# Optimization experiments

Measured on AMD Instinct MI355X. Metric: run time of the kernel, lower is better.

## Reference

```python
import jax, jax.numpy as jnp
import numpy as np

B, LQ, LK, E, H = 4, 2048, 2048, 768, 12
D = E // H  # head_dim = 64
SCALE = 0.25 / np.sqrt(D)
LN_EPS = 1e-5


def _layernorm(x, g, b):
    mu = jnp.mean(x, axis=-1, keepdims=True)
    var = jnp.mean(jnp.square(x - mu), axis=-1, keepdims=True)
    return (x - mu) * jax.lax.rsqrt(var + LN_EPS) * g + b


def _rope(x, f):
    # x: [B,H,L,D]; f: [L,D//2,2] (real, imag) -- complex multiply on interleaved pairs
    xr = x.reshape(*x.shape[:-1], D // 2, 2)
    fr = f[None, None]  # [1,1,L,D//2,2]
    real = xr[..., 0] * fr[..., 0] - xr[..., 1] * fr[..., 1]
    imag = xr[..., 0] * fr[..., 1] + xr[..., 1] * fr[..., 0]
    return jnp.stack([real, imag], axis=-1).reshape(x.shape)


def setup_inputs() -> dict:
    key = jax.random.key(0)
    ks = jax.random.split(key, 8)
    x_q = jax.random.normal(ks[0], (B, LQ, E), jnp.float32)
    x_kv = jax.random.normal(ks[1], (B, LK, E), jnp.float32)
    # unit-magnitude rotary tables (cos, sin of random angles)
    ang_q = jax.random.uniform(ks[2], (LQ, D // 2), jnp.float32, 0.0, 2 * np.pi)
    ang_k = jax.random.uniform(ks[3], (LK, D // 2), jnp.float32, 0.0, 2 * np.pi)
    freqs_cis = jnp.stack([jnp.cos(ang_q), jnp.sin(ang_q)], axis=-1)
    freqs_cis_cross = jnp.stack([jnp.cos(ang_k), jnp.sin(ang_k)], axis=-1)
    Wq = jax.random.normal(ks[4], (E, E), jnp.float32) * 0.02
    Wkv = jax.random.normal(ks[5], (E, 2 * E), jnp.float32) * 0.02
    Wo = jax.random.normal(ks[6], (E, E), jnp.float32) * 0.02
    bo = jnp.zeros((E,), jnp.float32)
    return {
        'x_q': x_q, 'x_kv': x_kv,
        'freqs_cis': freqs_cis, 'freqs_cis_cross': freqs_cis_cross,
        'Wq': Wq, 'Wkv': Wkv, 'Wo': Wo, 'bo': bo,
        'ln_q_g': jnp.ones((E,), jnp.float32), 'ln_q_b': jnp.zeros((E,), jnp.float32),
        'ln_kv_g': jnp.ones((E,), jnp.float32), 'ln_kv_b': jnp.zeros((E,), jnp.float32),
        'gain': jnp.array(1.0, jnp.float32),
    }


def reference(x_q, x_kv, freqs_cis, freqs_cis_cross, Wq, Wkv, Wo, bo,
              ln_q_g, ln_q_b, ln_kv_g, ln_kv_b, gain):
    q = _layernorm(x_q, ln_q_g, ln_q_b) @ Wq                 # [B,LQ,E]
    kv = _layernorm(x_kv, ln_kv_g, ln_kv_b) @ Wkv            # [B,LK,2E]
    k, v = jnp.split(kv, 2, axis=-1)
    # b l (h d) -> b h l d
    q = q.reshape(B, LQ, H, D).transpose(0, 2, 1, 3)
    k = k.reshape(B, LK, H, D).transpose(0, 2, 1, 3)
    v = v.reshape(B, LK, H, D).transpose(0, 2, 1, 3)
    q = _rope(q, freqs_cis)
    k = _rope(k, freqs_cis_cross)
    attn = jnp.einsum('bhqd,bhkd->bhqk', q, k) * SCALE       # full O(L^2) matrix
    attn = jax.nn.softmax(attn, axis=-1)
    out = jnp.einsum('bhqk,bhkd->bhqd', attn, v)
    out = out.transpose(0, 2, 1, 3).reshape(B, LQ, E)        # b h l d -> b l (h d)
    return gain * (out @ Wo + bo)
```

## Files before the change

kernel.cpp:

```cpp
#include <hip/hip_runtime.h>
#include <hip/hip_bf16.h>

#define B_ 4
#define LQ_ 2048
#define LK_ 2048
#define E_ 768
#define H_ 12
#define D_ 64
#define SCALE_ 0.03125f
#define QSCALE_ 0.04508422f

using short8 = __attribute__((ext_vector_type(8))) short;
using f32x4  = __attribute__((ext_vector_type(4))) float;
using f32x16 = __attribute__((ext_vector_type(16))) float;

__device__ inline unsigned short f2bf(float f) {
    union { float f; unsigned u; } v; v.f = f;
    unsigned r = (v.u + 0x7FFFu + ((v.u >> 16) & 1u)) >> 16;
    return (unsigned short)r;
}

__device__ inline unsigned pkbf(float a, float b) {
    union { float f; unsigned u; } x, y; x.f = a; y.f = b;
    return ((x.u + 0x8000u) >> 16) | ((y.u + 0x8000u) & 0xffff0000u);
}

__device__ inline unsigned pkcvt(float a, float b) {
    float2 p; p.x = a; p.y = b;
    __hip_bfloat162 pb = __float22bfloat162_rn(p);
    union { __hip_bfloat162 h; unsigned u; } c; c.h = pb;
    return c.u;
}

__device__ inline void gll16(const void* g, void* l) {
    __builtin_amdgcn_global_load_lds(
        (const __attribute__((address_space(1))) unsigned int*)g,
        (__attribute__((address_space(3))) unsigned int*)l, 16, 0, 0);
}

__global__ __launch_bounds__(256) void ln_tr_kernel(
    const float* __restrict__ xq, const float* __restrict__ xkv,
    const float* __restrict__ gq, const float* __restrict__ bq,
    const float* __restrict__ gk, const float* __restrict__ bk,
    unsigned short* __restrict__ yq, unsigned short* __restrict__ ykv,
    const float* __restrict__ Wq, const float* __restrict__ Wkv, const float* __restrict__ Wo,
    unsigned short* __restrict__ WqT, unsigned short* __restrict__ WkvT, unsigned short* __restrict__ WoT)
{
    __shared__ float tile[32][33];
    int bid = blockIdx.x;
    if (bid < 4096) {
        int wave = threadIdx.x >> 6, lane = threadIdx.x & 63;
        int row = bid * 4 + wave;
        const float* x; const float* g; const float* be; unsigned short* y;
        if (row < 8192) { x = xq; g = gq; be = bq; y = yq; }
        else { row -= 8192; x = xkv; g = gk; be = bk; y = ykv; }
        const float* xr = x + (size_t)row * E_;
        float4 v[3];
        float s = 0.f;
#pragma unroll
        for (int i = 0; i < 3; i++) {
            v[i] = *(const float4*)(xr + i * 256 + lane * 4);
            s += v[i].x + v[i].y + v[i].z + v[i].w;
        }
#pragma unroll
        for (int off = 32; off >= 1; off >>= 1) s += __shfl_xor(s, off);
        float mu = s * (1.0f / E_);
        float q = 0.f;
#pragma unroll
        for (int i = 0; i < 3; i++) {
            float dx = v[i].x - mu, dy = v[i].y - mu, dz = v[i].z - mu, dw = v[i].w - mu;
            q += dx * dx + dy * dy + dz * dz + dw * dw;
        }
#pragma unroll
        for (int off = 32; off >= 1; off >>= 1) q += __shfl_xor(q, off);
        float rstd = rsqrtf(q * (1.0f / E_) + 1e-5f);
        unsigned short* yr = y + (size_t)row * E_;
#pragma unroll
        for (int i = 0; i < 3; i++) {
            int c = i * 256 + lane * 4;
            float4 gv = *(const float4*)(g + c);
            float4 bv = *(const float4*)(be + c);
            ushort4 o;
            o.x = f2bf((v[i].x - mu) * rstd * gv.x + bv.x);
            o.y = f2bf((v[i].y - mu) * rstd * gv.y + bv.y);
            o.z = f2bf((v[i].z - mu) * rstd * gv.z + bv.z);
            o.w = f2bf((v[i].w - mu) * rstd * gv.w + bv.w);
            *(ushort4*)(yr + c) = o;
        }
        return;
    }
    int b2 = bid - 4096;
    int z = b2 / 1152;
    int rem = b2 - z * 1152;
    int bx = rem % 48, by = rem / 48;
    const float* in; unsigned short* out; int C;
    if (z == 0)      { in = Wq;  out = WqT;  C = E_; }
    else if (z == 1) { in = Wkv; out = WkvT; C = 2 * E_; }
    else             { in = Wo;  out = WoT;  C = E_; }
    int c0 = bx * 32, r0 = by * 32;
    if (c0 >= C) return;
    int tx = threadIdx.x & 31, ty = threadIdx.x >> 5;
#pragma unroll
    for (int i = 0; i < 32; i += 8)
        tile[ty + i][tx] = in[(size_t)(r0 + ty + i) * C + c0 + tx];
    __syncthreads();
#pragma unroll
    for (int i = 0; i < 32; i += 8)
        out[(size_t)(c0 + ty + i) * E_ + r0 + tx] = f2bf(tile[tx][ty + i]);
}

#define BN 128
#define BK 64
template<int BMT>
__device__ __forceinline__ void gemm_body(
    const unsigned short* __restrict__ A, const unsigned short* __restrict__ Bt,
    int K, int mode, int bm, int bn,
    unsigned short* __restrict__ outQ, const float* __restrict__ freqs,
    unsigned short* __restrict__ outK, unsigned short* __restrict__ outV,
    float* __restrict__ outF, const float* __restrict__ bo, const float* __restrict__ gain)
{
    constexpr int MT = (BMT == 128) ? 4 : 2;
    constexpr int SMEMN = (BMT == 128) ? 128 * 136 : (BMT * 64 + 128 * 64);
    __shared__ __align__(16) unsigned short smem[SMEMN];
    auto Asm = (unsigned short (*)[BK])smem;
    auto Bsm = (unsigned short (*)[BK])(smem + BMT * BK);

    int tid = threadIdx.x;
    int wave = tid >> 6, lane = tid & 63;
    int quad = lane >> 4, l16 = lane & 15;
    int waveM = (wave >> 1) * (MT * 16), waveN = (wave & 1) * 64;
    int ro = lane >> 3, cx = lane & 7;
    int sco = ((cx ^ ro) * 8);

    f32x4 acc[MT][4] = {};

    for (int k0 = 0; k0 < K; k0 += BK) {
        const unsigned short* Ag = A + (size_t)(bm + wave * (BMT / 4) + ro) * K + k0 + sco;
        const unsigned short* Bg = Bt + (size_t)(bn + wave * 32 + ro) * K + k0 + sco;
#pragma unroll
        for (int i = 0; i < BMT / 32; i++)
            gll16(Ag + (size_t)(i * 8) * K, &Asm[wave * (BMT / 4) + i * 8][0]);
#pragma unroll
        for (int i = 0; i < 4; i++)
            gll16(Bg + (size_t)(i * 8) * K, &Bsm[wave * 32 + i * 8][0]);
        __syncthreads();
#pragma unroll
        for (int kk = 0; kk < BK; kk += 32) {
            short8 fa[MT], fb[4];
#pragma unroll
            for (int t = 0; t < 4; t++) {
                int pos = ((quad + (kk >> 3)) ^ (l16 & 7)) * 8;
                if (t < MT) fa[t] = *(const short8*)(&Asm[waveM + t * 16 + l16][pos]);
                fb[t] = *(const short8*)(&Bsm[waveN + t * 16 + l16][pos]);
            }
#pragma unroll
            for (int mt = 0; mt < MT; mt++)
#pragma unroll
                for (int nt = 0; nt < 4; nt++)
                    acc[mt][nt] = __builtin_amdgcn_mfma_f32_16x16x32_bf16(fa[mt], fb[nt], acc[mt][nt], 0, 0, 0);
        }
        __syncthreads();
    }

    if (BMT == 128 && mode == 1 && bn >= E_) {
        auto T = (unsigned short (*)[136])smem;
#pragma unroll
        for (int mt = 0; mt < MT; mt++) {
#pragma unroll
            for (int nt = 0; nt < 4; nt++) {
                int ml = waveM + mt * 16 + quad * 4;
                int nl = waveN + nt * 16 + l16;
                *(unsigned*)&T[nl][ml]     = pkbf(acc[mt][nt][0], acc[mt][nt][1]);
                *(unsigned*)&T[nl][ml + 2] = pkbf(acc[mt][nt][2], acc[mt][nt][3]);
            }
        }
        __syncthreads();
        int nnbase = bn - E_;
        int bb = bm >> 11, l0 = bm & (LQ_ - 1);
#pragma unroll
        for (int it = 0; it < 8; it++) {
            int row = it * 16 + (tid >> 4);
            int hh = (nnbase + row) >> 6, dd = (nnbase + row) & 63;
            short8 v = *(const short8*)&T[row][(tid & 15) * 8];
            *(short8*)(outV + (((size_t)bb * H_ + hh) * D_ + dd) * LK_ + l0 + (tid & 15) * 8) = v;
        }
        return;
    }

    float gg = (mode == 2) ? gain[0] : 0.f;
#pragma unroll
    for (int mt = 0; mt < MT; mt++) {
#pragma unroll
        for (int nt = 0; nt < 4; nt++) {
#pragma unroll
            for (int r = 0; r < 4; r++) {
                int m = bm + waveM + mt * 16 + quad * 4 + r;
                int n = bn + waveN + nt * 16 + l16;
                float v = acc[mt][nt][r];
                if (mode == 2) {
                    outF[(size_t)m * E_ + n] = gg * (v + bo[n]);
                } else {
                    int l = m & (LQ_ - 1), bb = m >> 11;
                    float partner = __shfl_xor(v, 1);
                    int h = n >> 6, dd = n & 63;
                    const float* f = freqs + ((size_t)l * 32 + (dd >> 1)) * 2;
                    float f0 = f[0], f1 = f[1];
                    float o = ((dd & 1) == 0) ? (v * f0 - partner * f1)
                                              : (partner * f1 + v * f0);
                    if (mode == 0) o *= QSCALE_;
                    unsigned short* dst = (mode == 0) ? outQ : outK;
                    dst[(((size_t)bb * H_ + h) * LQ_ + l) * D_ + dd] = f2bf(o);
                }
            }
        }
    }
}

template<int BMT>
__global__ __launch_bounds__(256) void gemm_kernel(
    const unsigned short* __restrict__ A, const unsigned short* __restrict__ Bt,
    int K, int mode,
    unsigned short* __restrict__ outQ, const float* __restrict__ freqs,
    unsigned short* __restrict__ outK, unsigned short* __restrict__ outV,
    float* __restrict__ outF, const float* __restrict__ bo, const float* __restrict__ gain)
{
    gemm_body<BMT>(A, Bt, K, mode, blockIdx.x * BMT, blockIdx.y * BN,
                   outQ, freqs, outK, outV, outF, bo, gain);
}

__global__ __launch_bounds__(256) void proj_kernel(
    const unsigned short* __restrict__ xq_ln, const unsigned short* __restrict__ xkv_ln,
    const unsigned short* __restrict__ WqT, const unsigned short* __restrict__ WkvT,
    unsigned short* __restrict__ Qb, unsigned short* __restrict__ Kb,
    unsigned short* __restrict__ Vt,
    const float* __restrict__ freqs_q, const float* __restrict__ freqs_k)
{
    int bid = blockIdx.x;
    const unsigned short* A; const unsigned short* Bt; int mode, bm, bn;
    const float* fr; unsigned short* oQ; unsigned short* oK; unsigned short* oV;
    if (bid < 768) {
        int x = bid & 63, y = bid >> 6;
        A = xkv_ln; Bt = WkvT; mode = 1; bm = x * 128; bn = y * 128;
        fr = freqs_k; oQ = nullptr; oK = Kb; oV = Vt;
    } else {
        int b2 = bid - 768;
        int x = b2 & 63, y = b2 >> 6;
        A = xq_ln; Bt = WqT; mode = 0; bm = x * 128; bn = y * 128;
        fr = freqs_q; oQ = Qb; oK = nullptr; oV = nullptr;
    }
    gemm_body<128>(A, Bt, E_, mode, bm, bn, oQ, fr, oK, oV, nullptr, nullptr, nullptr);
}

__global__ __launch_bounds__(256, 4) void attn_kernel(
    const unsigned short* __restrict__ Qg, const unsigned short* __restrict__ Kg,
    const unsigned short* __restrict__ Vt, unsigned short* __restrict__ O)
{
    __shared__ unsigned short Ksm[3][64][64];
    __shared__ unsigned short Vsm[3][64][64];

    int tid = threadIdx.x;
    int wave = tid >> 6, lane = tid & 63;
    int l32 = lane & 31, hi = lane >> 5;
    int bh = blockIdx.x;
    int b = bh / H_, h = bh % H_;
    int qbase = blockIdx.y * 128 + wave * 32;

    const size_t head = (size_t)bh * LK_ * D_;
    const unsigned short* Qh = Qg + head;
    const unsigned short* Kh = Kg + head;
    const unsigned short* Vh = Vt + head;

    short8 qf[4];
#pragma unroll
    for (int dc = 0; dc < 4; dc++)
        qf[dc] = *(const short8*)(Qh + (size_t)(qbase + l32) * D_ + dc * 16 + hi * 8);

    f32x16 oacc[2] = {};
    float lsum = 0.f;

    int ro = lane >> 3, cx = lane & 7;
    int sco = ((cx ^ ro) * 8);
    int sw = l32 & 7;

    auto stage = [&](int t, int bf) {
        const unsigned short* Kp = Kh + (size_t)(t * 64 + wave * 16 + ro) * D_ + sco;
        const unsigned short* Vp = Vh + (size_t)(wave * 16 + ro) * LK_ + t * 64 + sco;
        gll16(Kp,            &Ksm[bf][wave * 16][0]);
        gll16(Kp + 8 * D_,   &Ksm[bf][wave * 16 + 8][0]);
        gll16(Vp,            &Vsm[bf][wave * 16][0]);
        gll16(Vp + 8 * LK_,  &Vsm[bf][wave * 16 + 8][0]);
    };

    auto compute = [&](int bf) {
        f32x16 st0 = {}, st1 = {};
        __builtin_amdgcn_s_setprio(1);
#pragma unroll
        for (int dc = 0; dc < 4; dc++) {
            int pos = ((dc * 2 + hi) ^ sw) * 8;
            short8 k0 = *(const short8*)(&Ksm[bf][l32][pos]);
            short8 k1 = *(const short8*)(&Ksm[bf][32 + l32][pos]);
            st0 = __builtin_amdgcn_mfma_f32_32x32x16_bf16(k0, qf[dc], st0, 0, 0, 0);
            st1 = __builtin_amdgcn_mfma_f32_32x32x16_bf16(k1, qf[dc], st1, 0, 0, 0);
        }
        __builtin_amdgcn_s_setprio(0);

        unsigned pks0[8], pks1[8];
#pragma unroll
        for (int t = 0; t < 8; t++) {
            float p0 = __builtin_amdgcn_exp2f(st0[2 * t]);
            float p1 = __builtin_amdgcn_exp2f(st0[2 * t + 1]);
            lsum += p0 + p1;
            pks0[t] = pkcvt(p0, p1);
        }
#pragma unroll
        for (int t = 0; t < 8; t++) {
            float p0 = __builtin_amdgcn_exp2f(st1[2 * t]);
            float p1 = __builtin_amdgcn_exp2f(st1[2 * t + 1]);
            lsum += p0 + p1;
            pks1[t] = pkcvt(p0, p1);
        }
        asm("v_permlane32_swap_b32 %0, %1" : "+v"(pks0[0]), "+v"(pks0[2]));
        asm("v_permlane32_swap_b32 %0, %1" : "+v"(pks0[1]), "+v"(pks0[3]));
        asm("v_permlane32_swap_b32 %0, %1" : "+v"(pks0[4]), "+v"(pks0[6]));
        asm("v_permlane32_swap_b32 %0, %1" : "+v"(pks0[5]), "+v"(pks0[7]));
        asm("v_permlane32_swap_b32 %0, %1" : "+v"(pks1[0]), "+v"(pks1[2]));
        asm("v_permlane32_swap_b32 %0, %1" : "+v"(pks1[1]), "+v"(pks1[3]));
        asm("v_permlane32_swap_b32 %0, %1" : "+v"(pks1[4]), "+v"(pks1[6]));
        asm("v_permlane32_swap_b32 %0, %1" : "+v"(pks1[5]), "+v"(pks1[7]));

        __builtin_amdgcn_s_setprio(1);
#pragma unroll
        for (int half = 0; half < 2; half++) {
#pragma unroll
            for (int kk = 0; kk < 2; kk++) {
                union { unsigned u[4]; short8 s8; } pf;
#pragma unroll
                for (int g = 0; g < 4; g++)
                    pf.u[g] = half ? pks1[kk * 4 + g] : pks0[kk * 4 + g];
#pragma unroll
                for (int dt = 0; dt < 2; dt++) {
                    int pos = (((half * 2 + kk) * 2 + hi) ^ sw) * 8;
                    short8 vfr = *(const short8*)(&Vsm[bf][dt * 32 + l32][pos]);
                    oacc[dt] = __builtin_amdgcn_mfma_f32_32x32x16_bf16(pf.s8, vfr, oacc[dt], 0, 0, 0);
                }
            }
        }
        __builtin_amdgcn_s_setprio(0);
    };

    stage(0, 0);
    stage(1, 1);
    asm volatile("s_waitcnt vmcnt(4)\ns_barrier" ::: "memory");

    for (int t = 0; t < 30; ++t) {
        stage(t + 2, (t + 2) % 3);
        compute(t % 3);
        asm volatile("s_waitcnt vmcnt(4) lgkmcnt(0)\ns_barrier" ::: "memory");
    }
    compute(0);
    asm volatile("s_waitcnt vmcnt(0) lgkmcnt(0)\ns_barrier" ::: "memory");
    compute(1);

    lsum += __shfl_xor(lsum, 32);
    float inv = 1.f / lsum;
#pragma unroll
    for (int reg = 0; reg < 16; reg++) {
        int ql = (reg & 3) + 8 * (reg >> 2) + 4 * hi;
        float iq = __shfl(inv, ql);
        int q = qbase + ql;
        size_t base = ((size_t)b * LQ_ + q) * E_ + h * D_;
#pragma unroll
        for (int dt = 0; dt < 2; dt++)
            O[base + dt * 32 + l32] = f2bf(oacc[dt][reg] * iq);
    }
}

extern "C" void kernel_launch(void* const* d_in, const int* in_sizes, int n_in,
                              void* d_out, int out_size, void* d_ws, size_t ws_size,
                              hipStream_t stream)
{
    const float* x_q     = (const float*)d_in[0];
    const float* x_kv    = (const float*)d_in[1];
    const float* freqs_q = (const float*)d_in[2];
    const float* freqs_k = (const float*)d_in[3];
    const float* Wq      = (const float*)d_in[4];
    const float* Wkv     = (const float*)d_in[5];
    const float* Wo      = (const float*)d_in[6];
    const float* bo      = (const float*)d_in[7];
    const float* ln_q_g  = (const float*)d_in[8];
    const float* ln_q_b  = (const float*)d_in[9];
    const float* ln_kv_g = (const float*)d_in[10];
    const float* ln_kv_b = (const float*)d_in[11];
    const float* gain    = (const float*)d_in[12];
    float* out = (float*)d_out;

    unsigned short* ws = (unsigned short*)d_ws;
    const size_t SZ = (size_t)B_ * LQ_ * E_;
    unsigned short* xq_ln  = ws;
    unsigned short* xkv_ln = xq_ln + SZ;
    unsigned short* Qb     = xkv_ln + SZ;
    unsigned short* Kb     = Qb + SZ;
    unsigned short* Vt     = Kb + SZ;
    unsigned short* Ob     = xq_ln;
    unsigned short* WqT    = Vt + SZ;
    unsigned short* WkvT   = WqT + E_ * E_;
    unsigned short* WoT    = WkvT + 2 * E_ * E_;

    ln_tr_kernel<<<7552, 256, 0, stream>>>(x_q, x_kv, ln_q_g, ln_q_b, ln_kv_g, ln_kv_b,
                                           xq_ln, xkv_ln, Wq, Wkv, Wo, WqT, WkvT, WoT);
    proj_kernel<<<1152, 256, 0, stream>>>(xq_ln, xkv_ln, WqT, WkvT, Qb, Kb, Vt,
                                          freqs_q, freqs_k);
    attn_kernel<<<dim3(48, 16), 256, 0, stream>>>(Qb, Kb, Vt, Ob);
    gemm_kernel<64><<<dim3(128, 6), 256, 0, stream>>>(Ob, WoT, E_, 2,
                                                      nullptr, nullptr, nullptr, nullptr, out, bo, gain);
}
```

Baseline: 254.5 us.

## Compute softmax row sums with an MFMA against ones and unroll the triple-buffer loop

Drops the per-element VALU accumulation of the softmax denominator. The row sum is now produced by one extra MFMA per P fragment, multiplying the bf16 P against a vector of ones, which also removes the final shuffles. The K-tile loop is unrolled by three so buffer indices become compile-time constants, and LDS read offsets are precomputed. This costs one extra MFMA per 4 and a 16-register accumulator, and the sum now uses bf16-rounded P, which is consistent with the P·V numerator.

```diff
diff --git a/kernel.cpp b/kernel.cpp
--- a/kernel.cpp
+++ b/kernel.cpp
@@ -13,6 +13,8 @@
 using short8 = __attribute__((ext_vector_type(8))) short;
 using f32x4  = __attribute__((ext_vector_type(4))) float;
 using f32x16 = __attribute__((ext_vector_type(16))) float;
+
+template<int N> struct IC { static constexpr int v = N; };
 
 __device__ inline unsigned short f2bf(float f) {
     union { float f; unsigned u; } v; v.f = f;
@@ -255,8 +257,7 @@
     const unsigned short* __restrict__ Qg, const unsigned short* __restrict__ Kg,
     const unsigned short* __restrict__ Vt, unsigned short* __restrict__ O)
 {
-    __shared__ unsigned short Ksm[3][64][64];
-    __shared__ unsigned short Vsm[3][64][64];
+    __shared__ __align__(16) unsigned short smem[3 * 4096 * 2];
 
     int tid = threadIdx.x;
     int wave = tid >> 6, lane = tid & 63;
@@ -276,29 +277,43 @@
         qf[dc] = *(const short8*)(Qh + (size_t)(qbase + l32) * D_ + dc * 16 + hi * 8);
 
     f32x16 oacc[2] = {};
-    float lsum = 0.f;
+    f32x16 lacc = {};
+
+    short8 ones;
+#pragma unroll
+    for (int i = 0; i < 8; i++) ones[i] = (short)0x3F80;
 
     int ro = lane >> 3, cx = lane & 7;
     int sco = ((cx ^ ro) * 8);
     int sw = l32 & 7;
-
-    auto stage = [&](int t, int bf) {
-        const unsigned short* Kp = Kh + (size_t)(t * 64 + wave * 16 + ro) * D_ + sco;
-        const unsigned short* Vp = Vh + (size_t)(wave * 16 + ro) * LK_ + t * 64 + sco;
-        gll16(Kp,            &Ksm[bf][wave * 16][0]);
-        gll16(Kp + 8 * D_,   &Ksm[bf][wave * 16 + 8][0]);
-        gll16(Vp,            &Vsm[bf][wave * 16][0]);
-        gll16(Vp + 8 * LK_,  &Vsm[bf][wave * 16 + 8][0]);
+    int hs = hi ^ sw;
+
+    unsigned bs[4];
+#pragma unroll
+    for (int c = 0; c < 4; c++)
+        bs[c] = l32 * 64 + (((c * 2) ^ hs) * 8);
+
+    const unsigned short* kst = Kh + (size_t)(wave * 16 + ro) * D_ + sco;
+    const unsigned short* vst = Vh + (size_t)(wave * 16 + ro) * LK_ + sco;
+
+    auto stage = [&](const unsigned short* Kp, const unsigned short* Vp, int bf) {
+        gll16(Kp,            &smem[bf * 4096 + (wave * 16) * 64]);
+        gll16(Kp + 8 * D_,   &smem[bf * 4096 + (wave * 16 + 8) * 64]);
+        gll16(Vp,            &smem[12288 + bf * 4096 + (wave * 16) * 64]);
+        gll16(Vp + 8 * LK_,  &smem[12288 + bf * 4096 + (wave * 16 + 8) * 64]);
     };
 
-    auto compute = [&](int bf) {
+    auto compute = [&](auto bfc) {
+        constexpr int bf = decltype(bfc)::v;
+        constexpr int KO = bf * 4096;
+        constexpr int VO = 12288 + bf * 4096;
+
         f32x16 st0 = {}, st1 = {};
         __builtin_amdgcn_s_setprio(1);
 #pragma unroll
         for (int dc = 0; dc < 4; dc++) {
-            int pos = ((dc * 2 + hi) ^ sw) * 8;
-            short8 k0 = *(const short8*)(&Ksm[bf][l32][pos]);
-            short8 k1 = *(const short8*)(&Ksm[bf][32 + l32][pos]);
+            short8 k0 = *(const short8*)&smem[bs[dc] + KO];
+            short8 k1 = *(const short8*)&smem[bs[dc] + KO + 2048];
             st0 = __builtin_amdgcn_mfma_f32_32x32x16_bf16(k0, qf[dc], st0, 0, 0, 0);
             st1 = __builtin_amdgcn_mfma_f32_32x32x16_bf16(k1, qf[dc], st1, 0, 0, 0);
         }
@@ -309,14 +324,12 @@
         for (int t = 0; t < 8; t++) {
             float p0 = __builtin_amdgcn_exp2f(st0[2 * t]);
             float p1 = __builtin_amdgcn_exp2f(st0[2 * t + 1]);
-            lsum += p0 + p1;
             pks0[t] = pkcvt(p0, p1);
         }
 #pragma unroll
         for (int t = 0; t < 8; t++) {
             float p0 = __builtin_amdgcn_exp2f(st1[2 * t]);
             float p1 = __builtin_amdgcn_exp2f(st1[2 * t + 1]);
-            lsum += p0 + p1;
             pks1[t] = pkcvt(p0, p1);
         }
         asm("v_permlane32_swap_b32 %0, %1" : "+v"(pks0[0]), "+v"(pks0[2]));
@@ -337,41 +350,47 @@
 #pragma unroll
                 for (int g = 0; g < 4; g++)
                     pf.u[g] = half ? pks1[kk * 4 + g] : pks0[kk * 4 + g];
+                constexpr int cbase = 0;
+                (void)cbase;
 #pragma unroll
                 for (int dt = 0; dt < 2; dt++) {
-                    int pos = (((half * 2 + kk) * 2 + hi) ^ sw) * 8;
-                    short8 vfr = *(const short8*)(&Vsm[bf][dt * 32 + l32][pos]);
+                    short8 vfr = *(const short8*)&smem[bs[half * 2 + kk] + VO + dt * 2048];
                     oacc[dt] = __builtin_amdgcn_mfma_f32_32x32x16_bf16(pf.s8, vfr, oacc[dt], 0, 0, 0);
                 }
+                lacc = __builtin_amdgcn_mfma_f32_32x32x16_bf16(pf.s8, ones, lacc, 0, 0, 0);
             }
         }
         __builtin_amdgcn_s_setprio(0);
     };
 
-    stage(0, 0);
-    stage(1, 1);
+    stage(kst, vst, 0);
+    stage(kst + 4096, vst + 64, 1);
     asm volatile("s_waitcnt vmcnt(4)\ns_barrier" ::: "memory");
 
-    for (int t = 0; t < 30; ++t) {
-        stage(t + 2, (t + 2) % 3);
-        compute(t % 3);
+    for (int it = 0; it < 10; ++it) {
+        int t = 3 * it;
+        stage(kst + (size_t)(t + 2) * 4096, vst + (size_t)(t + 2) * 64, 2);
+        compute(IC<0>{});
         asm volatile("s_waitcnt vmcnt(4) lgkmcnt(0)\ns_barrier" ::: "memory");
-    }
-    compute(0);
+        stage(kst + (size_t)(t + 3) * 4096, vst + (size_t)(t + 3) * 64, 0);
+        compute(IC<1>{});
+        asm volatile("s_waitcnt vmcnt(4) lgkmcnt(0)\ns_barrier" ::: "memory");
+        stage(kst + (size_t)(t + 4) * 4096, vst + (size_t)(t + 4) * 64, 1);
+        compute(IC<2>{});
+        asm volatile("s_waitcnt vmcnt(4) lgkmcnt(0)\ns_barrier" ::: "memory");
+    }
+    compute(IC<0>{});
     asm volatile("s_waitcnt vmcnt(0) lgkmcnt(0)\ns_barrier" ::: "memory");
-    compute(1);
-
-    lsum += __shfl_xor(lsum, 32);
-    float inv = 1.f / lsum;
+    compute(IC<1>{});
+
 #pragma unroll
     for (int reg = 0; reg < 16; reg++) {
         int ql = (reg & 3) + 8 * (reg >> 2) + 4 * hi;
-        float iq = __shfl(inv, ql);
         int q = qbase + ql;
+        float inv = 1.f / lacc[reg];
         size_t base = ((size_t)b * LQ_ + q) * E_ + h * D_;
-#pragma unroll
-        for (int dt = 0; dt < 2; dt++)
-            O[base + dt * 32 + l32] = f2bf(oacc[dt][reg] * iq);
+        O[base + l32]      = f2bf(oacc[0][reg] * inv);
+        O[base + 32 + l32] = f2bf(oacc[1][reg] * inv);
     }
 }
 
```

Measured after the change: 256.4 us. About the same (+0.7%).
